# Kernel optimization log

Measured on AMD Instinct MI355X. Metric: run time of the kernel, lower is better.

Reference implementation:

```python
import jax, jax.numpy as jnp
import numpy as np
jax.config.update('jax_enable_x64', True)

B, S, D, H, V, P = 4, 2048, 512, 8, 100000, 256
NGRAMS = list(range(3, 9))  # n-gram lengths 3..8
DH = D // H
SCALE = np.float32(DH ** -0.5)

def _layernorm(x, g, b, eps=1e-5):
    m = jnp.mean(x, -1, keepdims=True)
    v = jnp.mean(jnp.square(x - m), -1, keepdims=True)
    return g * (x - m) / jnp.sqrt(v + eps) + b

def _mha(q, k, v, Wq, bq, Wk, bk, Wv, bv, Wo, bo):
    Bq, Lq, _ = q.shape
    qh = (q @ Wq + bq).reshape(Bq, Lq, H, DH)
    kh = (k @ Wk + bk).reshape(Bq, -1, H, DH)
    vh = (v @ Wv + bv).reshape(Bq, -1, H, DH)
    s = jnp.einsum('bqhd,bkhd->bhqk', qh, kh) * SCALE
    a = jax.nn.softmax(s, axis=-1)
    o = jnp.einsum('bhqk,bkhd->bqhd', a, vh).reshape(Bq, Lq, D)
    return o @ Wo + bo

def _ngram_hash(bytes_seq, n):
    # hash[:, i] = sum_k bytes[:, i-n+1+k] * 256**k for i >= n-1 else 0, then mod V
    # (int64 wraparound for n=8 matches torch semantics)
    b = bytes_seq.astype(jnp.int64)
    h = jnp.zeros_like(b)
    for k in range(n):
        shift = n - 1 - k
        shifted = jnp.pad(b, ((0, 0), (shift, 0)))[:, :S]
        h = h + shifted * (256 ** k)
    h = jnp.where(jnp.arange(S) >= (n - 1), h, 0)
    return h % V

def _forward(bytes_seq, patch_idx, byte_emb, ngram_emb, sWq, sbq, sWk, sbk, sWv, sbv, sWo, sbo, ln1g, ln1b, W1, b1, W2, b2, ln2g, ln2b, cWq, cbq, cWk, cbk, cWv, cbv, cWo, cbo):
    embeds = byte_emb[bytes_seq]  # [B,S,D]
    for j, n in enumerate(NGRAMS):
        embeds = embeds + ngram_emb[j][_ngram_hash(bytes_seq, n)]
    embeds = embeds / np.float32(len(NGRAMS) + 1)
    # one post-norm transformer encoder layer (relu FFN, eval mode / no dropout)
    x = _layernorm(embeds + _mha(embeds, embeds, embeds, sWq, sbq, sWk, sbk, sWv, sbv, sWo, sbo), ln1g, ln1b)
    ff = jax.nn.relu(x @ W1 + b1) @ W2 + b2
    x = _layernorm(x + ff, ln2g, ln2b)
    # gather patch-boundary queries per batch, cross-attend to full sequence
    q = jnp.take_along_axis(x, patch_idx[..., None], axis=1)  # [B,P,D]
    return _mha(q, x, x, cWq, cbq, cWk, cbk, cWv, cbv, cWo, cbo)

def setup_inputs():
    key = jax.random.key(0)
    ks = jax.random.split(key, 20)
    f32 = jnp.float32
    def rn(k, shape, scale=0.02):
        return (jax.random.normal(k, shape, f32) * scale).astype(f32)
    return {
        'bytes_seq': jax.random.randint(ks[0], (B, S), 0, 256, dtype=jnp.int64),
        'patch_idx': jnp.sort(jax.random.randint(ks[1], (B, P), 0, S, dtype=jnp.int64), axis=1),
        'byte_emb': rn(ks[2], (256, D)),
        'ngram_emb': rn(ks[3], (len(NGRAMS), V, D)),
        'sWq': rn(ks[4], (D, D)), 'sbq': jnp.zeros((D,), f32),
        'sWk': rn(ks[5], (D, D)), 'sbk': jnp.zeros((D,), f32),
        'sWv': rn(ks[6], (D, D)), 'sbv': jnp.zeros((D,), f32),
        'sWo': rn(ks[7], (D, D)), 'sbo': jnp.zeros((D,), f32),
        'ln1g': jnp.ones((D,), f32), 'ln1b': jnp.zeros((D,), f32),
        'W1': rn(ks[8], (D, 4 * D)), 'b1': jnp.zeros((4 * D,), f32),
        'W2': rn(ks[9], (4 * D, D)), 'b2': jnp.zeros((D,), f32),
        'ln2g': jnp.ones((D,), f32), 'ln2b': jnp.zeros((D,), f32),
        'cWq': rn(ks[10], (D, D)), 'cbq': jnp.zeros((D,), f32),
        'cWk': rn(ks[11], (D, D)), 'cbk': jnp.zeros((D,), f32),
        'cWv': rn(ks[12], (D, D)), 'cbv': jnp.zeros((D,), f32),
        'cWo': rn(ks[13], (D, D)), 'cbo': jnp.zeros((D,), f32),
    }

def reference(bytes_seq, patch_idx, byte_emb, ngram_emb, sWq, sbq, sWk, sbk, sWv, sbv, sWo, sbo, ln1g, ln1b, W1, b1, W2, b2, ln2g, ln2b, cWq, cbq, cWk, cbk, cWv, cbv, cWo, cbo):
    return _forward(bytes_seq, patch_idx, byte_emb, ngram_emb, sWq, sbq, sWk, sbk, sWv, sbv, sWo, sbo, ln1g, ln1b, W1, b1, W2, b2, ln2g, ln2b, cWq, cbq, cWk, cbk, cWv, cbv, cWo, cbo)
```

## Files before the change

### kernel.cpp

```cpp
#include <hip/hip_runtime.h>
#include <stdint.h>

#define B_   4
#define S_   2048
#define D_   512
#define H_   8
#define DH_  64
#define V_   100000
#define P_   256
#define N_   (B_*S_)
#define NP_  (B_*P_)

typedef _Float16 f16;
typedef _Float16 f16x8 __attribute__((ext_vector_type(8)));
typedef float    f32x4 __attribute__((ext_vector_type(4)));
typedef uint32_t u32x4 __attribute__((ext_vector_type(4)));

#define MFMA16(a,b,c) __builtin_amdgcn_mfma_f32_16x16x32_f16((a),(b),(c),0,0,0)
#define GLDS16(gp, lp) __builtin_amdgcn_global_load_lds( \
    (const __attribute__((address_space(1))) void*)(gp), \
    (__attribute__((address_space(3))) void*)(lp), 16, 0, 0)

struct WJobs {
  const float* src[10];
  f16* dst[10];
  int K[10], N[10], tiles[10];
};

__global__ __launch_bounds__(256) void prep_kernel(WJobs jobs,
    const float* __restrict__ sbq, const float* __restrict__ sbk,
    const float* __restrict__ sbv, const float* __restrict__ cbk,
    const float* __restrict__ cbv, float* __restrict__ bqkv,
    float* __restrict__ bckv,
    const int* __restrict__ bytes_seq, const float* __restrict__ byte_emb,
    const float* __restrict__ ngram_emb, f16* __restrict__ out16)
{
  int bid = blockIdx.x;
  if (bid < 10240) {
    const int j = bid >> 10, tile = bid & 1023;
    if (tile >= jobs.tiles[j]) return;
    const int K = jobs.K[j], N = jobs.N[j];
    const int ntiles = N >> 5;
    const int kt = (tile / ntiles) << 5, nt = (tile % ntiles) << 5;
    __shared__ float T[32][33];
    const int t = threadIdx.x;
    const float* src = jobs.src[j];
    #pragma unroll
    for (int p = 0; p < 4; p++) {
      int lin = t + p * 256;
      int rr = lin >> 5, cc = lin & 31;
      T[rr][cc] = src[(size_t)(kt + rr) * N + nt + cc];
    }
    __syncthreads();
    f16* dst = jobs.dst[j];
    #pragma unroll
    for (int p = 0; p < 4; p++) {
      int lin = t + p * 256;
      int rr = lin >> 5, cc = lin & 31;
      dst[(size_t)(nt + rr) * K + kt + cc] = (f16)T[cc][rr];
    }
    return;
  }
  bid -= 10240;
  if (bid < 10) {
    int t = bid * 256 + threadIdx.x;
    if (t < 512)       bqkv[t] = sbq[t];
    else if (t < 1024) bqkv[t] = sbk[t - 512];
    else if (t < 1536) bqkv[t] = sbv[t - 1024];
    else if (t < 2048) bckv[t - 1536] = cbk[t - 1536];
    else if (t < 2560) bckv[t - 1536] = cbv[t - 2048];
    return;
  }
  bid -= 10;
  const int pos = bid * 2 + (threadIdx.x >> 7);
  const int b = pos / S_, s = pos % S_;
  const int* bs = bytes_seq + (size_t)b * S_;

  int w[8];
  #pragma unroll
  for (int k = 0; k < 8; k++) {
    int p = s - 7 + k;
    w[k] = (p >= 0) ? bs[p] : 0;
  }
  int idx[6];
  #pragma unroll
  for (int j = 0; j < 6; j++) {
    const int n = j + 3;
    int id = 0;
    if (s >= n - 1) {
      uint64_t h = 0;
      for (int k = 0; k < n; k++)
        h += (uint64_t)(uint32_t)w[8 - n + k] << (8 * k);
      long long sh = (long long)h;
      long long r = sh % (long long)V_;
      if (r < 0) r += V_;
      id = (int)r;
    }
    idx[j] = id;
  }
  const int d = (threadIdx.x & 127) * 4;
  float4 acc = *(const float4*)(byte_emb + (size_t)bs[s] * D_ + d);
  #pragma unroll
  for (int j = 0; j < 6; j++) {
    const float4 v = *(const float4*)(ngram_emb + ((size_t)j * V_ + idx[j]) * D_ + d);
    acc.x += v.x; acc.y += v.y; acc.z += v.z; acc.w += v.w;
  }
  const float inv7 = 1.0f / 7.0f;
  f16 t4[4];
  t4[0] = (f16)(acc.x * inv7); t4[1] = (f16)(acc.y * inv7);
  t4[2] = (f16)(acc.z * inv7); t4[3] = (f16)(acc.w * inv7);
  *(uint2*)(out16 + (size_t)pos * D_ + d) = *(uint2*)t4;
}

template<typename OutT, int RELU, int BN, int VTSTART, int K>
__device__ __forceinline__ void gemm_body(
    const f16* __restrict__ A, const f16* __restrict__ Bt,
    const float* __restrict__ bias, OutT* __restrict__ C,
    int N, const int* __restrict__ rowmap,
    f16* __restrict__ vt, int bmi, int bni, int lda, int ldb)
{
  constexpr int NF = BN / 32;
  constexpr int NT = K / 32;
  constexpr int U  = (NT < 8) ? NT : 8;
  __shared__ __align__(16) f16 As[2][128 * 32];
  __shared__ __align__(16) f16 Bs[2][BN * 32];
  const int tid = threadIdx.x;
  const int l = tid & 63;
  const int lo4 = l & 15, hi2 = l >> 4;
  const int w = tid >> 6;
  const int wr = w >> 1, wc = w & 1;
  const int bm = bmi * 128, bn = bni * BN;

  const f16* ap[2];
  #pragma unroll
  for (int i = 0; i < 2; i++) {
    int r = bm + i * 64 + (tid >> 2);
    int ar = rowmap ? ((r >> 8) * S_ + rowmap[r]) : r;
    ap[i] = A + (size_t)ar * lda + (tid & 3) * 8;
  }
  const f16* bp[BN / 64];
  #pragma unroll
  for (int i = 0; i < BN / 64; i++) {
    int c = i * 256 + tid;
    bp[i] = Bt + (size_t)(bn + (c >> 2)) * ldb + (tid & 3) * 8;
  }

  f32x4 acc[4][NF];
  #pragma unroll
  for (int m = 0; m < 4; m++)
    #pragma unroll
    for (int n = 0; n < NF; n++) acc[m][n] = (f32x4){0.f, 0.f, 0.f, 0.f};

  #pragma unroll
  for (int i = 0; i < 2; i++)
    GLDS16(ap[i], &As[0][(i * 256 + tid) * 8]);
  #pragma unroll
  for (int i = 0; i < BN / 64; i++)
    GLDS16(bp[i], &Bs[0][(i * 256 + tid) * 8]);

  for (int to = 0; to < NT / U; to++) {
    #pragma unroll
    for (int ti = 0; ti < U; ti++) {
      const int t = to * U + ti;
      __syncthreads();
      const int cur = t & 1;
      if (t + 1 < NT) {
        const int k0 = (t + 1) << 5;
        #pragma unroll
        for (int i = 0; i < 2; i++)
          GLDS16(ap[i] + k0, &As[cur ^ 1][(i * 256 + tid) * 8]);
        #pragma unroll
        for (int i = 0; i < BN / 64; i++)
          GLDS16(bp[i] + k0, &Bs[cur ^ 1][(i * 256 + tid) * 8]);
      }
      f16x8 af[4], bf[NF];
      const f16* pa = &As[cur][(wr * 64 + lo4) * 32 + hi2 * 8];
      const f16* pb = &Bs[cur][(wc * (BN / 2) + lo4) * 32 + hi2 * 8];
      #pragma unroll
      for (int m = 0; m < 4; m++) af[m] = *(const f16x8*)(pa + m * 16 * 32);
      #pragma unroll
      for (int n = 0; n < NF; n++) bf[n] = *(const f16x8*)(pb + n * 16 * 32);
      #pragma unroll
      for (int m = 0; m < 4; m++)
        #pragma unroll
        for (int n = 0; n < NF; n++)
          acc[m][n] = MFMA16(bf[n], af[m], acc[m][n]);
    }
  }

  if constexpr (VTSTART >= 0) {
    if (bn >= VTSTART) {
      #pragma unroll
      for (int n = 0; n < NF; n++) {
        const int col0 = bn + wc * (BN / 2) + n * 16 + hi2 * 4;
        float bb[4] = {0.f, 0.f, 0.f, 0.f};
        if (bias) *(float4*)bb = *(const float4*)(bias + col0);
        #pragma unroll
        for (int m = 0; m < 4; m++) {
          const int s = bm + wr * 64 + m * 16 + lo4;
          #pragma unroll
          for (int j = 0; j < 4; j++) {
            const int dcol = col0 + j - VTSTART;
            vt[(((size_t)(s >> 11) * 8 + (dcol >> 6)) << 17) +
               ((size_t)(dcol & 63) << 11) + (s & 2047)] =
                (f16)(acc[m][n][j] + bb[j]);
          }
        }
      }
      return;
    }
  }

  #pragma unroll
  for (int n = 0; n < NF; n++) {
    const int col0 = bn + wc * (BN / 2) + n * 16 + hi2 * 4;
    float bb[4] = {0.f, 0.f, 0.f, 0.f};
    if (bias) *(float4*)bb = *(const float4*)(bias + col0);
    #pragma unroll
    for (int m = 0; m < 4; m++) {
      const int row = bm + wr * 64 + m * 16 + lo4;
      float v[4];
      #pragma unroll
      for (int j = 0; j < 4; j++) {
        v[j] = acc[m][n][j] + bb[j];
        if (RELU) v[j] = fmaxf(v[j], 0.f);
      }
      if constexpr (sizeof(OutT) == 2) {
        f16 t4[4];
        #pragma unroll
        for (int j = 0; j < 4; j++) t4[j] = (f16)v[j];
        *(uint2*)((f16*)C + (size_t)row * N + col0) = *(uint2*)t4;
      } else {
        float4 t4 = {v[0], v[1], v[2], v[3]};
        *(float4*)((float*)C + (size_t)row * N + col0) = t4;
      }
    }
  }
}

template<typename OutT, int RELU, int BN, int VTSTART, int K>
__global__ __launch_bounds__(256) void gemm_f16(
    const f16* __restrict__ A, const f16* __restrict__ Bt,
    const float* __restrict__ bias, OutT* __restrict__ C,
    int N, const int* __restrict__ rowmap, f16* __restrict__ vt)
{
  gemm_body<OutT, RELU, BN, VTSTART, K>(A, Bt, bias, C, N, rowmap, vt,
                                        blockIdx.x, blockIdx.y, K, K);
}

__global__ __launch_bounds__(256) void ckv_cq_kernel(
    const f16* __restrict__ X, const f16* __restrict__ CKVT,
    const float* __restrict__ bckv, f16* __restrict__ CKV,
    f16* __restrict__ vt2, const f16* __restrict__ cWqT,
    const float* __restrict__ cbq, f16* __restrict__ CQ,
    const int* __restrict__ pidx)
{
  int bid = blockIdx.x;
  if (bid < 512) {
    gemm_body<f16, 0, 128, 512, 512>(X, CKVT, bckv, CKV, 1024,
                                     nullptr, vt2, bid >> 3, bid & 7, 512, 512);
  } else {
    bid -= 512;
    gemm_body<f16, 0, 64, -1, 512>(X, cWqT, cbq, CQ, 512,
                                   pidx, nullptr, bid >> 3, bid & 7, 512, 512);
  }
}

__global__ __launch_bounds__(256) void co_splitk(
    const f16* __restrict__ A, const f16* __restrict__ Bt,
    float* __restrict__ part)
{
  const int z = blockIdx.z;
  gemm_body<float, 0, 64, -1, 128>(A + z * 128, Bt + z * 128, nullptr,
      part + (size_t)z * NP_ * 512, 512, nullptr, nullptr,
      blockIdx.x, blockIdx.y, 512, 512);
}

__global__ __launch_bounds__(128) void co_reduce(
    const float* __restrict__ part, const float* __restrict__ bias,
    float* __restrict__ out)
{
  const int row = blockIdx.x;
  const int col = threadIdx.x * 4;
  float4 s = *(const float4*)(bias + col);
  #pragma unroll
  for (int c = 0; c < 4; c++) {
    const float4 v = *(const float4*)(part + ((size_t)c * NP_ + row) * 512 + col);
    s.x += v.x; s.y += v.y; s.z += v.z; s.w += v.w;
  }
  *(float4*)(out + (size_t)row * 512 + col) = s;
}

template<int QG, int CHUNKS>
__global__ __launch_bounds__(256) void attn_f16(
    const f16* __restrict__ Q, int qs,
    const f16* __restrict__ Kp, int kvs,
    const f16* __restrict__ VT, f16* __restrict__ O,
    float* __restrict__ Opart, float* __restrict__ Lpart, int NQ)
{
  constexpr int CL = S_ / CHUNKS;
  constexpr int NT = CL / 64;
  __shared__ __align__(16) f16 Ks[2][64][76];
  __shared__ __align__(16) f16 VtL[2][64 * 64];

  const int tid = threadIdx.x;
  const int w = tid >> 6, l = tid & 63;
  const int lo4 = l & 15, hi2 = l >> 4;
  const int lin = (CHUNKS == 1) ? blockIdx.x : (blockIdx.x & 127);
  const int c   = (CHUNKS == 1) ? 0 : (int)(blockIdx.x >> 7);
  const int h = lin & 7, b = (lin >> 3) & 3, qt = lin >> 5;

  const f16 qscale = (f16)0.18033688f;
  f16x8 qf[QG][2];
  #pragma unroll
  for (int qg = 0; qg < QG; qg++) {
    const int qrow = qt * (64 * QG) + w * (16 * QG) + qg * 16 + lo4;
    const f16* Qp = Q + (size_t)(b * NQ + qrow) * qs + h * DH_ + hi2 * 8;
    qf[qg][0] = *(const f16x8*)(Qp);
    qf[qg][1] = *(const f16x8*)(Qp + 32);
    #pragma unroll
    for (int i = 0; i < 8; i++) { qf[qg][0][i] *= qscale; qf[qg][1][i] *= qscale; }
  }

  const int g2 = lo4 >> 2, j4 = lo4 & 3;
  const int kvp0 = 8 * g2 + j4;
  const int kvp1 = 8 * (g2 ^ 2) + 4 + j4;
  const int pidx = (l ^ 32) << 2;
  const int vswz = lo4 & 7;

  const f16* Kb = Kp + ((size_t)b * S_ + c * CL) * kvs + h * DH_;
  const f16* VTbh = VT + (((size_t)(b * 8 + h)) << 17) + c * CL;

  float lsum[QG];
  f32x4 oacc[QG][4];
  #pragma unroll
  for (int qg = 0; qg < QG; qg++) {
    lsum[qg] = 0.f;
    #pragma unroll
    for (int df = 0; df < 4; df++) oacc[qg][df] = (f32x4){0.f, 0.f, 0.f, 0.f};
  }

  const int r0 = tid >> 3;
  const int c8 = tid & 7;

  #pragma unroll
  for (int i = 0; i < 2; i++) {
    int r = i * 32 + r0;
    GLDS16(VTbh + (size_t)r * 2048 + ((c8 ^ (r & 7)) * 8), &VtL[0][(i * 256 + tid) * 8]);
  }
  f16x8 kreg[2];
  #pragma unroll
  for (int i = 0; i < 2; i++)
    kreg[i] = *(const f16x8*)(Kb + (size_t)(i * 32 + r0) * kvs + c8 * 8);
  #pragma unroll
  for (int i = 0; i < 2; i++)
    *(f16x8*)(&Ks[0][i * 32 + r0][c8 * 8]) = kreg[i];
  __syncthreads();

  int cur = 0;
  for (int t = 0; t < NT; t++) {
    if (t + 1 < NT) {
      const int kt2 = (t + 1) * 64;
      #pragma unroll
      for (int i = 0; i < 2; i++) {
        int r = i * 32 + r0;
        GLDS16(VTbh + (size_t)r * 2048 + kt2 + ((c8 ^ (r & 7)) * 8),
               &VtL[cur ^ 1][(i * 256 + tid) * 8]);
      }
      #pragma unroll
      for (int i = 0; i < 2; i++)
        kreg[i] = *(const f16x8*)(Kb + (size_t)(kt2 + i * 32 + r0) * kvs + c8 * 8);
    }
    f32x4 sacc[QG][4];
    #pragma unroll
    for (int nf = 0; nf < 4; nf++) {
      const int krow = ((nf & 1) ? kvp1 : kvp0) + (nf >> 1) * 32;
      f16x8 kf0 = *(const f16x8*)(&Ks[cur][krow][hi2 * 8]);
      f16x8 kf1 = *(const f16x8*)(&Ks[cur][krow][32 + hi2 * 8]);
      #pragma unroll
      for (int qg = 0; qg < QG; qg++) {
        f32x4 s = (f32x4){0.f, 0.f, 0.f, 0.f};
        s = MFMA16(kf0, qf[qg][0], s);
        s = MFMA16(kf1, qf[qg][1], s);
        sacc[qg][nf] = s;
      }
    }
    uint32_t packs[QG][4][2];
    #pragma unroll
    for (int qg = 0; qg < QG; qg++)
      #pragma unroll
      for (int nf = 0; nf < 4; nf++) {
        float p0 = exp2f(sacc[qg][nf][0]);
        float p1 = exp2f(sacc[qg][nf][1]);
        float p2 = exp2f(sacc[qg][nf][2]);
        float p3 = exp2f(sacc[qg][nf][3]);
        lsum[qg] += (p0 + p1) + (p2 + p3);
        packs[qg][nf][0] = __builtin_bit_cast(uint32_t, __builtin_amdgcn_cvt_pkrtz(p0, p1));
        packs[qg][nf][1] = __builtin_bit_cast(uint32_t, __builtin_amdgcn_cvt_pkrtz(p2, p3));
      }
    #pragma unroll
    for (int ks = 0; ks < 2; ks++) {
      f16x8 pb[QG];
      #pragma unroll
      for (int qg = 0; qg < QG; qg++) {
        uint32_t w0 = packs[qg][2 * ks][0];
        uint32_t w1 = packs[qg][2 * ks][1];
        uint32_t w2 = (uint32_t)__builtin_amdgcn_ds_bpermute(pidx, (int)packs[qg][2 * ks + 1][0]);
        uint32_t w3 = (uint32_t)__builtin_amdgcn_ds_bpermute(pidx, (int)packs[qg][2 * ks + 1][1]);
        u32x4 bw = (u32x4){w0, w1, w2, w3};
        pb[qg] = __builtin_bit_cast(f16x8, bw);
      }
      #pragma unroll
      for (int df = 0; df < 4; df++) {
        const int r = df * 16 + lo4;
        const int cc = (ks * 4 + hi2) ^ vswz;
        f16x8 vf = *(const f16x8*)(&VtL[cur][r * 64 + cc * 8]);
        #pragma unroll
        for (int qg = 0; qg < QG; qg++)
          oacc[qg][df] = MFMA16(vf, pb[qg], oacc[qg][df]);
      }
    }
    if (t + 1 < NT) {
      #pragma unroll
      for (int i = 0; i < 2; i++)
        *(f16x8*)(&Ks[cur ^ 1][i * 32 + r0][c8 * 8]) = kreg[i];
    }
    __syncthreads();
    cur ^= 1;
  }

  #pragma unroll
  for (int qg = 0; qg < QG; qg++) {
    float r = lsum[qg];
    r += __shfl_xor(r, 16, 64);
    r += __shfl_xor(r, 32, 64);
    const int orow = qt * (64 * QG) + w * (16 * QG) + qg * 16 + lo4;
    if constexpr (CHUNKS == 1) {
      const float invl = 1.0f / r;
      f16* Ob = O + (size_t)(b * NQ + orow) * D_ + h * DH_ + hi2 * 4;
      #pragma unroll
      for (int df = 0; df < 4; df++) {
        f16 t4[4];
        #pragma unroll
        for (int j = 0; j < 4; j++) t4[j] = (f16)(oacc[qg][df][j] * invl);
        *(uint2*)(Ob + df * 16) = *(uint2*)t4;
      }
    } else {
      float* Op = Opart + ((size_t)c * NP_ + b * NQ + orow) * D_ + h * DH_ + hi2 * 4;
      #pragma unroll
      for (int df = 0; df < 4; df++) {
        float4 v = {oacc[qg][df][0], oacc[qg][df][1], oacc[qg][df][2], oacc[qg][df][3]};
        *(float4*)(Op + df * 16) = v;
      }
      if (hi2 == 0)
        Lpart[((size_t)c * NP_ + b * NQ + orow) * H_ + h] = r;
    }
  }
}

__global__ __launch_bounds__(128) void attn_reduce(
    const float* __restrict__ Opart, const float* __restrict__ Lpart,
    f16* __restrict__ CO)
{
  const int row = blockIdx.x;
  const int col = threadIdx.x * 4;
  const int h = col >> 6;
  float4 o = {0.f, 0.f, 0.f, 0.f};
  float ls = 0.f;
  #pragma unroll
  for (int c = 0; c < 4; c++) {
    const float4 v = *(const float4*)(Opart + ((size_t)c * NP_ + row) * D_ + col);
    o.x += v.x; o.y += v.y; o.z += v.z; o.w += v.w;
    ls += Lpart[((size_t)c * NP_ + row) * H_ + h];
  }
  const float inv = 1.0f / ls;
  f16 t4[4];
  t4[0] = (f16)(o.x * inv); t4[1] = (f16)(o.y * inv);
  t4[2] = (f16)(o.z * inv); t4[3] = (f16)(o.w * inv);
  *(uint2*)(CO + (size_t)row * D_ + col) = *(uint2*)t4;
}

__global__ __launch_bounds__(256) void ln_kernel(
    const f16* __restrict__ a, const f16* __restrict__ r,
    const float* __restrict__ g, const float* __restrict__ be,
    f16* __restrict__ out)
{
  const int row = blockIdx.x * 2 + (threadIdx.x >> 7);
  const int t = threadIdx.x & 127;
  const f16* ap = a + (size_t)row * D_ + t * 4;
  const f16* rp = r + (size_t)row * D_ + t * 4;
  uint2 au = *(const uint2*)ap, ru = *(const uint2*)rp;
  f16 a4[4], r4[4];
  *(uint2*)a4 = au; *(uint2*)r4 = ru;
  float x0 = (float)a4[0] + (float)r4[0];
  float x1 = (float)a4[1] + (float)r4[1];
  float x2 = (float)a4[2] + (float)r4[2];
  float x3 = (float)a4[3] + (float)r4[3];
  float sm = x0 + x1 + x2 + x3;
  float sq = x0*x0 + x1*x1 + x2*x2 + x3*x3;
  #pragma unroll
  for (int off = 32; off > 0; off >>= 1) {
    sm += __shfl_down(sm, off, 64);
    sq += __shfl_down(sq, off, 64);
  }
  __shared__ float s0[4], s1[4];
  if ((threadIdx.x & 63) == 0) { s0[threadIdx.x >> 6] = sm; s1[threadIdx.x >> 6] = sq; }
  __syncthreads();
  const int base = (threadIdx.x >> 7) * 2;
  const float Sm = s0[base] + s0[base + 1];
  const float Sq = s1[base] + s1[base + 1];
  const float mean = Sm * (1.0f / 512.0f);
  const float var  = Sq * (1.0f / 512.0f) - mean * mean;
  const float inv  = rsqrtf(var + 1e-5f);
  const float4 vg = *(const float4*)(g + t * 4);
  const float4 vb = *(const float4*)(be + t * 4);
  f16 o4[4];
  o4[0] = (f16)(vg.x * (x0 - mean) * inv + vb.x);
  o4[1] = (f16)(vg.y * (x1 - mean) * inv + vb.y);
  o4[2] = (f16)(vg.z * (x2 - mean) * inv + vb.z);
  o4[3] = (f16)(vg.w * (x3 - mean) * inv + vb.w);
  *(uint2*)(out + (size_t)row * D_ + t * 4) = *(uint2*)o4;
}

extern "C" void kernel_launch(void* const* d_in, const int* in_sizes, int n_in,
                              void* d_out, int out_size, void* d_ws, size_t ws_size,
                              hipStream_t stream) {
  const int*   bytes_seq = (const int*)  d_in[0];
  const int*   patch_idx = (const int*)  d_in[1];
  const float* byte_emb  = (const float*)d_in[2];
  const float* ngram_emb = (const float*)d_in[3];
  const float* sWq = (const float*)d_in[4];  const float* sbq = (const float*)d_in[5];
  const float* sWk = (const float*)d_in[6];  const float* sbk = (const float*)d_in[7];
  const float* sWv = (const float*)d_in[8];  const float* sbv = (const float*)d_in[9];
  const float* sWo = (const float*)d_in[10]; const float* sbo = (const float*)d_in[11];
  const float* ln1g = (const float*)d_in[12]; const float* ln1b = (const float*)d_in[13];
  const float* W1 = (const float*)d_in[14];  const float* b1 = (const float*)d_in[15];
  const float* W2 = (const float*)d_in[16];  const float* b2 = (const float*)d_in[17];
  const float* ln2g = (const float*)d_in[18]; const float* ln2b = (const float*)d_in[19];
  const float* cWq = (const float*)d_in[20]; const float* cbq = (const float*)d_in[21];
  const float* cWk = (const float*)d_in[22]; const float* cbk = (const float*)d_in[23];
  const float* cWv = (const float*)d_in[24]; const float* cbv = (const float*)d_in[25];
  const float* cWo = (const float*)d_in[26]; const float* cbo = (const float*)d_in[27];

  char* base = (char*)d_ws;
  const size_t MB = 1u << 20;
  f16* E16     = (f16*)(base + 0 * MB);
  f16* TMP16   = (f16*)(base + 8 * MB);
  f16* X116    = (f16*)(base + 16 * MB);
  f16* X216    = (f16*)(base + 24 * MB);
  f16* QKV16   = (f16*)(base + 32 * MB);
  f16* AT16    = (f16*)(base + 56 * MB);
  f16* HID16   = (f16*)(base + 64 * MB);
  f16* CKV16   = (f16*)(base + 96 * MB);
  f16* CQ16    = (f16*)(base + 112 * MB);
  f16* CO16    = (f16*)(base + 113 * MB);
  f16* WT      = (f16*)(base + 114 * MB);
  float* bqkv  = (float*)(base + 123 * MB);
  float* bckv  = bqkv + 1536;
  f16* VT      = (f16*)(base + 124 * MB);
  f16* VT2     = (f16*)(base + 132 * MB);
  float* OPART = (float*)(base + 140 * MB);
  float* LPART = (float*)(base + 148 * MB);

  f16* QKVT = WT;
  f16* sWoT = QKVT + 786432;
  f16* W1T  = sWoT + 262144;
  f16* W2T  = W1T + 1048576;
  f16* cWqT = W2T + 1048576;
  f16* CKVT = cWqT + 262144;
  f16* cWoT = CKVT + 524288;

  WJobs wj;
  {
    const float* wsrc[10] = {sWq, sWk, sWv, sWo, W1, W2, cWq, cWk, cWv, cWo};
    f16* wdst[10] = {QKVT, QKVT + 262144, QKVT + 524288, sWoT, W1T, W2T,
                     cWqT, CKVT, CKVT + 262144, cWoT};
    const int wK[10] = {512,512,512,512, 512,2048, 512,512,512,512};
    const int wN[10] = {512,512,512,512, 2048,512, 512,512,512,512};
    for (int i = 0; i < 10; i++) {
      wj.src[i] = wsrc[i]; wj.dst[i] = wdst[i];
      wj.K[i] = wK[i]; wj.N[i] = wN[i];
      wj.tiles[i] = (wK[i] >> 5) * (wN[i] >> 5);
    }
  }

  const dim3 blk256(256), blk128(128);

  prep_kernel<<<10240 + 10 + 4096, blk256, 0, stream>>>(
      wj, sbq, sbk, sbv, cbk, cbv, bqkv, bckv,
      bytes_seq, byte_emb, ngram_emb, E16);

  gemm_f16<f16, 0, 128, 1024, 512><<<dim3(64, 12), blk256, 0, stream>>>(
      E16, QKVT, bqkv, QKV16, 1536, nullptr, VT);

  attn_f16<2, 1><<<512, blk256, 0, stream>>>(
      QKV16, 1536, QKV16 + 512, 1536, VT, AT16, nullptr, nullptr, S_);

  gemm_f16<f16, 0, 64, -1, 512><<<dim3(64, 8), blk256, 0, stream>>>(
      AT16, sWoT, sbo, TMP16, 512, nullptr, nullptr);
  ln_kernel<<<N_/2, blk256, 0, stream>>>(E16, TMP16, ln1g, ln1b, X116);

  gemm_f16<f16, 1, 128, -1, 512><<<dim3(64, 16), blk256, 0, stream>>>(
      X116, W1T, b1, HID16, 2048, nullptr, nullptr);
  gemm_f16<f16, 0, 64, -1, 2048><<<dim3(64, 8), blk256, 0, stream>>>(
      HID16, W2T, b2, TMP16, 512, nullptr, nullptr);
  ln_kernel<<<N_/2, blk256, 0, stream>>>(X116, TMP16, ln2g, ln2b, X216);

  ckv_cq_kernel<<<576, blk256, 0, stream>>>(
      X216, CKVT, bckv, CKV16, VT2, cWqT, cbq, CQ16, patch_idx);
  attn_f16<1, 4><<<512, blk256, 0, stream>>>(
      CQ16, 512, CKV16, 1024, VT2, nullptr, OPART, LPART, P_);
  attn_reduce<<<NP_, blk128, 0, stream>>>(OPART, LPART, CO16);

  co_splitk<<<dim3(8, 8, 4), blk256, 0, stream>>>(CO16, cWoT, OPART);
  co_reduce<<<NP_, blk128, 0, stream>>>(OPART, cbo, (float*)d_out);
}
```

Before: 277.3 us.

## Triple-buffer GEMM LDS tiles with partial vmcnt waits for deeper prefetch

Replaces the double-buffered GEMM main loop with a three-stage LDS ring that prefetches two K-tiles ahead. Each iteration waits only until the older tile's global-to-LDS loads have landed (partial s_waitcnt vmcnt) before the barrier, so more memory latency overlaps with MFMA work. This uses 1.5x the shared memory, which may reduce occupancy, and it relies on hand-written waitcnt values that match the exact number of loads in flight.

```diff
diff --git a/kernel.cpp b/kernel.cpp
--- a/kernel.cpp
+++ b/kernel.cpp
@@ -20,6 +20,16 @@
 #define GLDS16(gp, lp) __builtin_amdgcn_global_load_lds( \
     (const __attribute__((address_space(1))) void*)(gp), \
     (__attribute__((address_space(3))) void*)(lp), 16, 0, 0)
+
+template<int N>
+__device__ __forceinline__ void wait_barrier() {
+  if constexpr (N == 0)
+    asm volatile("s_waitcnt vmcnt(0)\ns_barrier" ::: "memory");
+  else if constexpr (N == 3)
+    asm volatile("s_waitcnt vmcnt(3)\ns_barrier" ::: "memory");
+  else
+    asm volatile("s_waitcnt vmcnt(4)\ns_barrier" ::: "memory");
+}
 
 struct WJobs {
   const float* src[10];
@@ -121,9 +131,9 @@
 {
   constexpr int NF = BN / 32;
   constexpr int NT = K / 32;
-  constexpr int U  = (NT < 8) ? NT : 8;
-  __shared__ __align__(16) f16 As[2][128 * 32];
-  __shared__ __align__(16) f16 Bs[2][BN * 32];
+  constexpr int GL = 2 + BN / 64;
+  __shared__ __align__(16) f16 As[3][128 * 32];
+  __shared__ __align__(16) f16 Bs[3][BN * 32];
   const int tid = threadIdx.x;
   const int l = tid & 63;
   const int lo4 = l & 15, hi2 = l >> 4;
@@ -157,36 +167,47 @@
   #pragma unroll
   for (int i = 0; i < BN / 64; i++)
     GLDS16(bp[i], &Bs[0][(i * 256 + tid) * 8]);
-
-  for (int to = 0; to < NT / U; to++) {
-    #pragma unroll
-    for (int ti = 0; ti < U; ti++) {
-      const int t = to * U + ti;
-      __syncthreads();
-      const int cur = t & 1;
-      if (t + 1 < NT) {
-        const int k0 = (t + 1) << 5;
-        #pragma unroll
-        for (int i = 0; i < 2; i++)
-          GLDS16(ap[i] + k0, &As[cur ^ 1][(i * 256 + tid) * 8]);
-        #pragma unroll
-        for (int i = 0; i < BN / 64; i++)
-          GLDS16(bp[i] + k0, &Bs[cur ^ 1][(i * 256 + tid) * 8]);
-      }
-      f16x8 af[4], bf[NF];
-      const f16* pa = &As[cur][(wr * 64 + lo4) * 32 + hi2 * 8];
-      const f16* pb = &Bs[cur][(wc * (BN / 2) + lo4) * 32 + hi2 * 8];
-      #pragma unroll
-      for (int m = 0; m < 4; m++) af[m] = *(const f16x8*)(pa + m * 16 * 32);
-      #pragma unroll
-      for (int n = 0; n < NF; n++) bf[n] = *(const f16x8*)(pb + n * 16 * 32);
-      #pragma unroll
-      for (int m = 0; m < 4; m++)
-        #pragma unroll
-        for (int n = 0; n < NF; n++)
-          acc[m][n] = MFMA16(bf[n], af[m], acc[m][n]);
-    }
-  }
+  #pragma unroll
+  for (int i = 0; i < 2; i++)
+    GLDS16(ap[i] + 32, &As[1][(i * 256 + tid) * 8]);
+  #pragma unroll
+  for (int i = 0; i < BN / 64; i++)
+    GLDS16(bp[i] + 32, &Bs[1][(i * 256 + tid) * 8]);
+
+  auto do_mma = [&](int c) {
+    f16x8 af[4], bf[NF];
+    const f16* pa = &As[c][(wr * 64 + lo4) * 32 + hi2 * 8];
+    const f16* pb = &Bs[c][(wc * (BN / 2) + lo4) * 32 + hi2 * 8];
+    #pragma unroll
+    for (int m = 0; m < 4; m++) af[m] = *(const f16x8*)(pa + m * 16 * 32);
+    #pragma unroll
+    for (int n = 0; n < NF; n++) bf[n] = *(const f16x8*)(pb + n * 16 * 32);
+    #pragma unroll
+    for (int m = 0; m < 4; m++)
+      #pragma unroll
+      for (int n = 0; n < NF; n++)
+        acc[m][n] = MFMA16(bf[n], af[m], acc[m][n]);
+  };
+
+  int cur = 0;
+  #pragma unroll 3
+  for (int t = 0; t < NT - 1; ++t) {
+    wait_barrier<GL>();
+    if (t + 2 < NT) {
+      const int k0 = (t + 2) << 5;
+      int stg = cur + 2; if (stg >= 3) stg -= 3;
+      #pragma unroll
+      for (int i = 0; i < 2; i++)
+        GLDS16(ap[i] + k0, &As[stg][(i * 256 + tid) * 8]);
+      #pragma unroll
+      for (int i = 0; i < BN / 64; i++)
+        GLDS16(bp[i] + k0, &Bs[stg][(i * 256 + tid) * 8]);
+    }
+    do_mma(cur);
+    cur = (cur == 2) ? 0 : cur + 1;
+  }
+  wait_barrier<0>();
+  do_mma(cur);
 
   if constexpr (VTSTART >= 0) {
     if (bn >= VTSTART) {
```

Result: no change. 276.4 us (-0.3%).
